# Optimization experiments

Hardware: AMD Instinct MI355X
Metric: run time of the kernel (lower is better)

Reference implementation:

```python
import jax, jax.numpy as jnp
import numpy as np

K = 3          # conv kernel size
G = 3          # KAN grid intervals
SPLINE_K = 3   # B-spline order
N_BASIS = G + SPLINE_K  # 6


def extended_grid():
    # pykan-style grid on [-1, 1] with G intervals, extended by k knots each side
    h = 2.0 / G
    return jnp.arange(-SPLINE_K, G + SPLINE_K + 1, dtype=jnp.float32) * h - 1.0  # [G+2k+1]


def bspline_basis(x, t, k):
    """Cox-de Boor recursion. x: [...], t: [m] knots -> [..., m-1-k] bases."""
    x = x[..., None]
    b = ((x >= t[:-1]) & (x < t[1:])).astype(x.dtype)  # degree 0: [..., m-1]
    for d in range(1, k + 1):
        left = (x - t[: -(d + 1)]) / (t[d:-1] - t[: -(d + 1)]) * b[..., :-1]
        right = (t[d + 1:] - x) / (t[d + 1:] - t[1:-d]) * b[..., 1:]
        b = left + right
    return b  # [..., m-1-k]


def setup_inputs() -> dict:
    key = jax.random.key(0)
    k1, k2, k3, k4 = jax.random.split(key, 4)
    B, C, H, W = 32, 16, 64, 64
    in_dim, out_dim = C * K * K, 64
    x = jax.random.normal(k1, (B, C, H, W), dtype=jnp.float32)
    coef = jax.random.normal(k2, (in_dim, out_dim, N_BASIS), dtype=jnp.float32) * 0.1
    scale_base = jax.random.normal(k3, (in_dim, out_dim), dtype=jnp.float32) * (1.0 / np.sqrt(in_dim))
    scale_sp = jnp.ones((in_dim, out_dim), dtype=jnp.float32) + 0.0 * jax.random.normal(k4, (in_dim, out_dim))
    return {"x": x, "coef": coef, "scale_base": scale_base, "scale_sp": scale_sp}


def reference(x, coef, scale_base, scale_sp):
    B, C, H, W = x.shape
    Ho, Wo = H - K + 1, W - K + 1
    # im2col with torch-reshape ordering: feature index = c*K*K + di*K + dj
    cols = [x[:, :, di:di + Ho, dj:dj + Wo] for di in range(K) for dj in range(K)]
    patches = jnp.stack(cols, axis=2)                    # [B, C, K*K, Ho, Wo]
    patches = patches.reshape(B, C * K * K, Ho, Wo)      # [B, D, Ho, Wo]
    p = patches.transpose(0, 2, 3, 1)                    # [B, Ho, Wo, D]

    t = extended_grid()
    basis = bspline_basis(p, t, SPLINE_K)                # [B, Ho, Wo, D, N_BASIS]
    # spline part: sum over input dims and bases, with per-edge scale_sp folded into coef
    spline = jnp.einsum('bhwdn,don->bhwo', basis, coef * scale_sp[:, :, None])
    base = jnp.einsum('bhwd,do->bhwo', jax.nn.silu(p), scale_base)
    y = base + spline                                    # [B, Ho, Wo, O]
    return y.transpose(0, 3, 1, 2)                       # [B, O, Ho, Wo]
```

## Files before the change

kernel.cpp:

```cpp
#include <hip/hip_runtime.h>
#include <math.h>

#define Bsz 32
#define Cc  16
#define Hh  64
#define Ww  64
#define HO  62
#define WO  62
#define OD  64
#define ND  144
#define KC  18

using short8 = __attribute__((ext_vector_type(8))) short;
using f32x4  = __attribute__((ext_vector_type(4))) float;
using f32x16 = __attribute__((ext_vector_type(16))) float;
typedef unsigned int u32;
typedef unsigned short ushort;

__device__ __forceinline__ ushort f2bf(float f) {
    union { float f; unsigned u; } v; v.f = f;
    unsigned r = v.u + 0x7fff + ((v.u >> 16) & 1);
    return (ushort)(r >> 16);
}
__device__ __forceinline__ float bf2f(ushort h) {
    union { unsigned u; float f; } v; v.u = ((unsigned)h) << 16; return v.f;
}

__device__ __forceinline__ void gload_lds16(const void* g, void* l) {
    __builtin_amdgcn_global_load_lds((const __attribute__((address_space(1))) u32*)g,
                                     (__attribute__((address_space(3))) u32*)l,
                                     16, 0, 0);
}

__device__ __forceinline__ uint4 feat_pack(float xv) {
    float xi = (xv + 3.0f) * 1.5f;
    float fi = floorf(xi);
    int   ii = (int)fi;
    float u  = xi - fi;
    float u2 = u * u, u3 = u2 * u;
    float P0 = u3 * (1.0f / 6.0f);
    float P1 = (1.0f + 3.0f * u + 3.0f * u2 - 3.0f * u3) * (1.0f / 6.0f);
    float P2 = (4.0f - 6.0f * u2 + 3.0f * u3) * (1.0f / 6.0f);
    float om = 1.0f - u;
    float P3 = om * om * om * (1.0f / 6.0f);
    bool ok = (ii >= 0) && (ii <= 8);
    float bas[6];
    #pragma unroll
    for (int n = 0; n < 6; ++n) {
        int t = ii - n;
        float v = (t == 0) ? P0 : (t == 1) ? P1 : (t == 2) ? P2 : (t == 3) ? P3 : 0.0f;
        bas[n] = ok ? v : 0.0f;
    }
    float s = xv / (1.0f + __expf(-xv));
    ushort sh = f2bf(s);
    ushort sl = f2bf(s - bf2f(sh));
    uint4 pk;
    pk.x = (unsigned)f2bf(bas[0]) | ((unsigned)f2bf(bas[1]) << 16);
    pk.y = (unsigned)f2bf(bas[2]) | ((unsigned)f2bf(bas[3]) << 16);
    pk.z = (unsigned)f2bf(bas[4]) | ((unsigned)f2bf(bas[5]) << 16);
    pk.w = (unsigned)sh | ((unsigned)sl << 16);
    return pk;
}

__global__ __launch_bounds__(256) void kan_feat(const float* __restrict__ x,
                                                uint4* __restrict__ fg) {
    int base = blockIdx.x * 2048 + threadIdx.x;
    #pragma unroll
    for (int j = 0; j < 8; ++j) {
        int i = base + j * 256;
        fg[i] = feat_pack(x[i]);
    }
}

__global__ __launch_bounds__(256) void kan_prep3(const float* __restrict__ coef,
                                                 const float* __restrict__ sbase,
                                                 const float* __restrict__ ssp,
                                                 ushort* __restrict__ wpb) {
    int g = blockIdx.x * 256 + threadIdx.x;
    if (g >= KC * 8 * 64) return;
    int n = g & 63, d = g >> 6;
    float sspv = ssp[d * OD + n];
    ushort sb = f2bf(sbase[d * OD + n]);
    ushort v[8];
    #pragma unroll
    for (int f = 0; f < 6; ++f) v[f] = f2bf(coef[(d * OD + n) * 6 + f] * sspv);
    v[6] = sb; v[7] = sb;
    uint4 pk;
    pk.x = (unsigned)v[0] | ((unsigned)v[1] << 16);
    pk.y = (unsigned)v[2] | ((unsigned)v[3] << 16);
    pk.z = (unsigned)v[4] | ((unsigned)v[5] << 16);
    pk.w = (unsigned)v[6] | ((unsigned)v[7] << 16);
    *(uint4*)&wpb[(size_t)g * 8] = pk;
}

__global__ __launch_bounds__(256, 3) void kan_gemm2(const uint4* __restrict__ fg,
                                                    const uint4* __restrict__ wpb,
                                                    float* __restrict__ out) {
    __shared__ uint4 ldsmem[3072];
    char* lds = (char*)ldsmem;

    const int tid  = threadIdx.x;
    const int wid  = tid >> 6;
    const int lane = tid & 63;
    const int l31  = lane & 31;
    const int hi   = lane >> 5;
    const int mt   = blockIdx.x;
    const int bb   = blockIdx.y;
    const int h0   = mt * 2;

    auto stage = [&](int kc, int bufsel) {
        char* bufA = lds + bufsel * 24576;
        char* bufB = bufA + 16384;
        #pragma unroll
        for (int q = 0; q < 2; ++q) {
            int s = wid + q * 4;
            int d = kc * 8 + s;
            int c   = (d * 57) >> 9;
            int rem = d - c * 9;
            int di  = (rem * 11) >> 5;
            int dj  = rem - di * 3;
            int su  = c * 4096 + (h0 + di) * 64 + dj;
            #pragma unroll
            for (int hh = 0; hh < 2; ++hh) {
                const char* src = (const char*)fg +
                    ((size_t)(bb * 65536 + su + hh * 64 + lane) * 16);
                gload_lds16(src, bufA + (s * 128 + hh * 64) * 16);
            }
        }
        #pragma unroll
        for (int q = 0; q < 2; ++q) {
            int kb = wid + q * 4;
            const char* src = (const char*)wpb + ((size_t)(kc * 512 + kb * 64 + lane) * 16);
            gload_lds16(src, bufB + kb * 1024);
        }
    };

    f32x16 acc0, acc1;
    #pragma unroll
    for (int i = 0; i < 16; ++i) { acc0[i] = 0.0f; acc1[i] = 0.0f; }

    stage(0, 0);
    __syncthreads();

    const int m0 = wid * 32 + l31;

    #pragma unroll
    for (int kc = 0; kc < KC; ++kc) {
        const int cur = kc & 1;
        if (kc + 1 < KC) stage(kc + 1, cur ^ 1);
        const ushort* A  = (const ushort*)(lds + cur * 24576);
        const ushort* Bw = (const ushort*)(lds + cur * 24576 + 16384);
        #pragma unroll
        for (int kk = 0; kk < 4; ++kk) {
            const int sl = kk * 2 + hi;
            short8 a  = *(const short8*)(A  + (size_t)(sl * 128 + m0) * 8);
            short8 b0 = *(const short8*)(Bw + (size_t)(sl * 64 + l31) * 8);
            short8 b1 = *(const short8*)(Bw + (size_t)(sl * 64 + 32 + l31) * 8);
            acc0 = __builtin_amdgcn_mfma_f32_32x32x16_bf16(a, b0, acc0, 0, 0, 0);
            acc1 = __builtin_amdgcn_mfma_f32_32x32x16_bf16(a, b1, acc1, 0, 0, 0);
        }
        __syncthreads();
    }

    float* Csc = (float*)lds;
    #pragma unroll
    for (int r = 0; r < 16; ++r) {
        int ml = (r & 3) + ((r >> 2) << 3) + (hi << 2);
        Csc[(size_t)l31 * 130 + wid * 32 + ml]        = acc0[r];
        Csc[(size_t)(32 + l31) * 130 + wid * 32 + ml] = acc1[r];
    }
    __syncthreads();
    #pragma unroll
    for (int it = 0; it < 16; ++it) {
        int flat = it * 256 + tid;
        int o = flat >> 6, hh = (flat >> 5) & 1, fc = flat & 31;
        if (fc < 31) {
            float2 v = *(float2*)&Csc[(size_t)o * 130 + hh * 64 + fc * 2];
            *(float2*)&out[((size_t)(bb * OD + o) * HO + h0 + hh) * WO + fc * 2] = v;
        }
    }
}

#define NCHUNK 36
#define FW 68
__global__ __launch_bounds__(256) void kan_prep(const float* __restrict__ coef,
                                                const float* __restrict__ sbase,
                                                const float* __restrict__ ssp,
                                                ushort* __restrict__ wp) {
    int idx = blockIdx.x * 256 + threadIdx.x;
    if (idx >= ND * OD * 8) return;
    int n = idx & 7, o = (idx >> 3) & 63, d = idx >> 9;
    float v = (n < 6) ? coef[(d * OD + o) * 6 + n] * ssp[d * OD + o] : sbase[d * OD + o];
    wp[idx] = f2bf(v);
}

__global__ __launch_bounds__(128) void kan_mfma(const float* __restrict__ x,
                                                const ushort* __restrict__ wp,
                                                float* __restrict__ out) {
    __shared__ uint4 feat[Cc * 4 * FW];
    const int rp = blockIdx.x, b = blockIdx.y, tid = threadIdx.x;
    const int wid = tid >> 6, lane = tid & 63, l15 = lane & 15, ks = lane >> 4;
    const int hrow0 = rp * 2;
    for (int i = tid; i < Cc * 4 * FW; i += 128) {
        int wl = i % FW, cr = i / FW, r = cr & 3, c = cr >> 2;
        int col = wl < Ww ? wl : Ww - 1;
        feat[i] = feat_pack(x[((b * Cc + c) * Hh + hrow0 + r) * Ww + col]);
    }
    __syncthreads();
    f32x4 acc[4][4];
    #pragma unroll
    for (int rt = 0; rt < 4; ++rt)
        #pragma unroll
        for (int ct = 0; ct < 4; ++ct) acc[rt][ct] = (f32x4){0.f, 0.f, 0.f, 0.f};
    auto loadA = [&](int chunk, short8* A) {
        int d = chunk * 4 + ks;
        int c = (d * 57) >> 9;
        int rem = d - c * 9;
        int di = (rem * 11) >> 5;
        int dj = rem - di * 3;
        const short8* ap = (const short8*)&feat[(c * 4 + wid + di) * FW + l15 + dj];
        A[0] = ap[0]; A[1] = ap[16]; A[2] = ap[32]; A[3] = ap[48];
    };
    auto loadB = [&](int chunk, short8* Bf) {
        int d = chunk * 4 + ks;
        const short8* bp = (const short8*)wp + (d * 64 + l15);
        Bf[0] = bp[0]; Bf[1] = bp[16]; Bf[2] = bp[32]; Bf[3] = bp[48];
    };
    short8 A0[4], B0[4], A1[4], B1[4];
    loadA(0, A0); loadB(0, B0);
    for (int cb = 0; cb < NCHUNK; cb += 2) {
        loadA(cb + 1, A1); loadB(cb + 1, B1);
        #pragma unroll
        for (int rt = 0; rt < 4; ++rt)
            #pragma unroll
            for (int ct = 0; ct < 4; ++ct)
                acc[rt][ct] = __builtin_amdgcn_mfma_f32_16x16x32_bf16(A0[rt], B0[ct], acc[rt][ct], 0, 0, 0);
        if (cb + 2 < NCHUNK) { loadA(cb + 2, A0); loadB(cb + 2, B0); }
        #pragma unroll
        for (int rt = 0; rt < 4; ++rt)
            #pragma unroll
            for (int ct = 0; ct < 4; ++ct)
                acc[rt][ct] = __builtin_amdgcn_mfma_f32_16x16x32_bf16(A1[rt], B1[ct], acc[rt][ct], 0, 0, 0);
    }
    __syncthreads();
    float* sC = ((float*)feat) + wid * (OD * FW);
    #pragma unroll
    for (int rt = 0; rt < 4; ++rt)
        #pragma unroll
        for (int ct = 0; ct < 4; ++ct)
            *(f32x4*)&sC[(ct * 16 + l15) * FW + rt * 16 + ks * 4] = acc[rt][ct];
    const int orow = hrow0 + wid;
    for (int j = 0; j < OD; ++j) {
        float v = sC[j * FW + lane];
        if (lane < WO) out[((b * OD + j) * HO + orow) * WO + lane] = v;
    }
}

extern "C" void kernel_launch(void* const* d_in, const int* in_sizes, int n_in,
                              void* d_out, int out_size, void* d_ws, size_t ws_size,
                              hipStream_t stream) {
    (void)in_sizes; (void)n_in; (void)out_size;
    const float* x     = (const float*)d_in[0];
    const float* coef  = (const float*)d_in[1];
    const float* sbase = (const float*)d_in[2];
    const float* ssp   = (const float*)d_in[3];
    float* out = (float*)d_out;

    const size_t wpb_bytes = (size_t)KC * 512 * 16;
    const size_t fg_bytes  = (size_t)Bsz * Cc * Hh * Ww * 16;
    const size_t need = wpb_bytes + fg_bytes + 4096;

    if (ws_size >= need) {
        uint4* wpb = (uint4*)d_ws;
        uint4* fg  = (uint4*)((char*)d_ws + wpb_bytes);
        kan_feat<<<1024, 256, 0, stream>>>(x, fg);
        kan_prep3<<<36, 256, 0, stream>>>(coef, sbase, ssp, (ushort*)wpb);
        dim3 grid(31, Bsz);
        kan_gemm2<<<grid, 256, 0, stream>>>(fg, wpb, out);
    } else if (ws_size >= (size_t)ND * OD * 8 * 2) {
        ushort* wp = (ushort*)d_ws;
        kan_prep<<<(ND * OD * 8 + 255) / 256, 256, 0, stream>>>(coef, sbase, ssp, wp);
        dim3 grid(HO / 2, Bsz);
        kan_mfma<<<grid, 128, 0, stream>>>(x, wp, out);
    }
}
```

Measured before the change: 51.99 us.

## Fuse B-spline feature computation into GEMM kernel via LDS, stream weights from registers

Removes the separate feature kernel, which wrote a 16-byte packed feature per input element to global memory (about 33 MB) that the GEMM then re-read. Each block now computes packed features for its 4 input rows x 16 channels directly into LDS and builds the im2col A operand from LDS with computed offsets. Weights are reordered in the prep kernel to match the new K ordering and are double-buffered in registers straight from global memory instead of LDS. This trades global traffic for redundant feature computation (each row is computed twice across neighbouring blocks) and more register pressure.

```diff
diff --git a/kernel.cpp b/kernel.cpp
--- a/kernel.cpp
+++ b/kernel.cpp
@@ -10,6 +10,7 @@
 #define OD  64
 #define ND  144
 #define KC  18
+#define FEAT_U4 (4096 + 16)
 
 using short8 = __attribute__((ext_vector_type(8))) short;
 using f32x4  = __attribute__((ext_vector_type(4))) float;
@@ -24,12 +25,6 @@
 }
 __device__ __forceinline__ float bf2f(ushort h) {
     union { unsigned u; float f; } v; v.u = ((unsigned)h) << 16; return v.f;
-}
-
-__device__ __forceinline__ void gload_lds16(const void* g, void* l) {
-    __builtin_amdgcn_global_load_lds((const __attribute__((address_space(1))) u32*)g,
-                                     (__attribute__((address_space(3))) u32*)l,
-                                     16, 0, 0);
 }
 
 __device__ __forceinline__ uint4 feat_pack(float xv) {
@@ -62,23 +57,17 @@
     return pk;
 }
 
-__global__ __launch_bounds__(256) void kan_feat(const float* __restrict__ x,
-                                                uint4* __restrict__ fg) {
-    int base = blockIdx.x * 2048 + threadIdx.x;
-    #pragma unroll
-    for (int j = 0; j < 8; ++j) {
-        int i = base + j * 256;
-        fg[i] = feat_pack(x[i]);
-    }
-}
-
-__global__ __launch_bounds__(256) void kan_prep3(const float* __restrict__ coef,
+__global__ __launch_bounds__(256) void kan_prep4(const float* __restrict__ coef,
                                                  const float* __restrict__ sbase,
                                                  const float* __restrict__ ssp,
                                                  ushort* __restrict__ wpb) {
     int g = blockIdx.x * 256 + threadIdx.x;
     if (g >= KC * 8 * 64) return;
-    int n = g & 63, d = g >> 6;
+    int n = g & 63, slot = g >> 6;
+    int kc = slot >> 3, sl = slot & 7, kk = sl >> 1, par = sl & 1;
+    int p = kc * 4 + kk;
+    int a = p / 9, rem = p - a * 9;
+    int d = (2 * a + par) * 9 + rem;
     float sspv = ssp[d * OD + n];
     ushort sb = f2bf(sbase[d * OD + n]);
     ushort v[8];
@@ -93,11 +82,10 @@
     *(uint4*)&wpb[(size_t)g * 8] = pk;
 }
 
-__global__ __launch_bounds__(256, 3) void kan_gemm2(const uint4* __restrict__ fg,
-                                                    const uint4* __restrict__ wpb,
-                                                    float* __restrict__ out) {
-    __shared__ uint4 ldsmem[3072];
-    char* lds = (char*)ldsmem;
+__global__ __launch_bounds__(256) void kan_fused(const float* __restrict__ x,
+                                                 const uint4* __restrict__ wpb,
+                                                 float* __restrict__ out) {
+    __shared__ uint4 feat[FEAT_U4];
 
     const int tid  = threadIdx.x;
     const int wid  = tid >> 6;
@@ -108,61 +96,53 @@
     const int bb   = blockIdx.y;
     const int h0   = mt * 2;
 
-    auto stage = [&](int kc, int bufsel) {
-        char* bufA = lds + bufsel * 24576;
-        char* bufB = bufA + 16384;
-        #pragma unroll
-        for (int q = 0; q < 2; ++q) {
-            int s = wid + q * 4;
-            int d = kc * 8 + s;
-            int c   = (d * 57) >> 9;
-            int rem = d - c * 9;
-            int di  = (rem * 11) >> 5;
-            int dj  = rem - di * 3;
-            int su  = c * 4096 + (h0 + di) * 64 + dj;
+    #pragma unroll
+    for (int j = 0; j < 16; ++j) {
+        int i = tid + j * 256;
+        int c = i >> 8, r = (i >> 6) & 3, w = i & 63;
+        float xv = x[(size_t)bb * 65536 + c * 4096 + (h0 + r) * 64 + w];
+        feat[i] = feat_pack(xv);
+    }
+    __syncthreads();
+
+    f32x16 acc0, acc1;
+    #pragma unroll
+    for (int i = 0; i < 16; ++i) { acc0[i] = 0.0f; acc1[i] = 0.0f; }
+
+    const int m0 = wid * 32 + l31;
+    const int hh = m0 >> 6, w = m0 & 63;
+    const short8* abase = (const short8*)feat + (hi * 256 + hh * 64 + w);
+    const uint4* bbase = wpb + hi * 64 + l31;
+
+    short8 bfr[2][8];
+    #pragma unroll
+    for (int kk = 0; kk < 4; ++kk) {
+        bfr[0][kk * 2 + 0] = *(const short8*)(bbase + (kk * 2) * 64);
+        bfr[0][kk * 2 + 1] = *(const short8*)(bbase + (kk * 2) * 64 + 32);
+    }
+
+    #pragma unroll
+    for (int kc = 0; kc < KC; ++kc) {
+        const int cur = kc & 1;
+        if (kc + 1 < KC) {
             #pragma unroll
-            for (int hh = 0; hh < 2; ++hh) {
-                const char* src = (const char*)fg +
-                    ((size_t)(bb * 65536 + su + hh * 64 + lane) * 16);
-                gload_lds16(src, bufA + (s * 128 + hh * 64) * 16);
+            for (int kk = 0; kk < 4; ++kk) {
+                bfr[cur ^ 1][kk * 2 + 0] = *(const short8*)(bbase + ((kc + 1) * 8 + kk * 2) * 64);
+                bfr[cur ^ 1][kk * 2 + 1] = *(const short8*)(bbase + ((kc + 1) * 8 + kk * 2) * 64 + 32);
             }
         }
         #pragma unroll
-        for (int q = 0; q < 2; ++q) {
-            int kb = wid + q * 4;
-            const char* src = (const char*)wpb + ((size_t)(kc * 512 + kb * 64 + lane) * 16);
-            gload_lds16(src, bufB + kb * 1024);
+        for (int kk = 0; kk < 4; ++kk) {
+            const int p = kc * 4 + kk;
+            const int a = p / 9, rem = p - a * 9, di = rem / 3, dj = rem - di * 3;
+            short8 av = abase[512 * a + 64 * di + dj];
+            acc0 = __builtin_amdgcn_mfma_f32_32x32x16_bf16(av, bfr[cur][kk * 2 + 0], acc0, 0, 0, 0);
+            acc1 = __builtin_amdgcn_mfma_f32_32x32x16_bf16(av, bfr[cur][kk * 2 + 1], acc1, 0, 0, 0);
         }
-    };
-
-    f32x16 acc0, acc1;
-    #pragma unroll
-    for (int i = 0; i < 16; ++i) { acc0[i] = 0.0f; acc1[i] = 0.0f; }
-
-    stage(0, 0);
-    __syncthreads();
-
-    const int m0 = wid * 32 + l31;
-
-    #pragma unroll
-    for (int kc = 0; kc < KC; ++kc) {
-        const int cur = kc & 1;
-        if (kc + 1 < KC) stage(kc + 1, cur ^ 1);
-        const ushort* A  = (const ushort*)(lds + cur * 24576);
-        const ushort* Bw = (const ushort*)(lds + cur * 24576 + 16384);
-        #pragma unroll
-        for (int kk = 0; kk < 4; ++kk) {
-            const int sl = kk * 2 + hi;
-            short8 a  = *(const short8*)(A  + (size_t)(sl * 128 + m0) * 8);
-            short8 b0 = *(const short8*)(Bw + (size_t)(sl * 64 + l31) * 8);
-            short8 b1 = *(const short8*)(Bw + (size_t)(sl * 64 + 32 + l31) * 8);
-            acc0 = __builtin_amdgcn_mfma_f32_32x32x16_bf16(a, b0, acc0, 0, 0, 0);
-            acc1 = __builtin_amdgcn_mfma_f32_32x32x16_bf16(a, b1, acc1, 0, 0, 0);
-        }
-        __syncthreads();
-    }
-
-    float* Csc = (float*)lds;
+    }
+
+    __syncthreads();
+    float* Csc = (float*)feat;
     #pragma unroll
     for (int r = 0; r < 16; ++r) {
         int ml = (r & 3) + ((r >> 2) << 3) + (hi << 2);
@@ -173,10 +153,10 @@
     #pragma unroll
     for (int it = 0; it < 16; ++it) {
         int flat = it * 256 + tid;
-        int o = flat >> 6, hh = (flat >> 5) & 1, fc = flat & 31;
+        int o = flat >> 6, hh2 = (flat >> 5) & 1, fc = flat & 31;
         if (fc < 31) {
-            float2 v = *(float2*)&Csc[(size_t)o * 130 + hh * 64 + fc * 2];
-            *(float2*)&out[((size_t)(bb * OD + o) * HO + h0 + hh) * WO + fc * 2] = v;
+            float2 v = *(float2*)&Csc[(size_t)o * 130 + hh2 * 64 + fc * 2];
+            *(float2*)&out[((size_t)(bb * OD + o) * HO + h0 + hh2) * WO + fc * 2] = v;
         }
     }
 }
@@ -266,17 +246,13 @@
     const float* ssp   = (const float*)d_in[3];
     float* out = (float*)d_out;
 
-    const size_t wpb_bytes = (size_t)KC * 512 * 16;
-    const size_t fg_bytes  = (size_t)Bsz * Cc * Hh * Ww * 16;
-    const size_t need = wpb_bytes + fg_bytes + 4096;
-
-    if (ws_size >= need) {
+    const size_t wpb_bytes = (size_t)KC * 8 * 64 * 16;
+
+    if (ws_size >= wpb_bytes + 4096) {
         uint4* wpb = (uint4*)d_ws;
-        uint4* fg  = (uint4*)((char*)d_ws + wpb_bytes);
-        kan_feat<<<1024, 256, 0, stream>>>(x, fg);
-        kan_prep3<<<36, 256, 0, stream>>>(coef, sbase, ssp, (ushort*)wpb);
+        kan_prep4<<<36, 256, 0, stream>>>(coef, sbase, ssp, (ushort*)wpb);
         dim3 grid(31, Bsz);
-        kan_gemm2<<<grid, 256, 0, stream>>>(fg, wpb, out);
+        kan_fused<<<grid, 256, 0, stream>>>(x, wpb, out);
     } else if (ws_size >= (size_t)ND * OD * 8 * 2) {
         ushort* wp = (ushort*)d_ws;
         kan_prep<<<(ND * OD * 8 + 255) / 256, 256, 0, stream>>>(coef, sbase, ssp, wp);
```

Result: slower. 70.40 us (+35.4%).
